# Kernel tuning notes

Measured on AMD Instinct MI355X. Metric: run time of the kernel, lower is better.

## Reference

```python
import jax, jax.numpy as jnp
import numpy as np

B, S, D, H = 4, 2048, 128, 8

def setup_inputs() -> dict:
    key = jax.random.key(0)
    ks = jax.random.split(key, 11)
    sc_in = 1.0 / np.sqrt(D)
    sc_out = 1.0 / np.sqrt(H * D)
    return {
        "Q": jax.random.normal(ks[0], (B, S, D), jnp.float32),
        "K": jax.random.normal(ks[1], (B, S, D), jnp.float32),
        "V": jax.random.normal(ks[2], (B, S, D), jnp.float32),
        "WQ_w": jax.random.normal(ks[3], (H * D, D), jnp.float32) * sc_in,
        "WQ_b": jax.random.normal(ks[4], (H * D,), jnp.float32) * 0.01,
        "WK_w": jax.random.normal(ks[5], (H * D, D), jnp.float32) * sc_in,
        "WK_b": jax.random.normal(ks[6], (H * D,), jnp.float32) * 0.01,
        "WV_w": jax.random.normal(ks[7], (H * D, D), jnp.float32) * sc_in,
        "WV_b": jax.random.normal(ks[8], (H * D,), jnp.float32) * 0.01,
        "W_w": jax.random.normal(ks[9], (D, H * D), jnp.float32) * sc_out,
        "W_b": jax.random.normal(ks[10], (D,), jnp.float32) * 0.01,
    }

def reference(Q, K, V, WQ_w, WQ_b, WK_w, WK_b, WV_w, WV_b, W_w, W_b):
    b, s, d = Q.shape
    h = WQ_w.shape[0] // d
    # Linear projections: [b,s,d] -> [b,s,h*d] -> [b,h,s,d]
    rQ = (Q @ WQ_w.T + WQ_b).reshape(b, s, h, d).transpose(0, 2, 1, 3)
    rK = (K @ WK_w.T + WK_b).reshape(b, s, h, d).transpose(0, 2, 1, 3)
    rV = (V @ WV_w.T + WV_b).reshape(b, s, h, d).transpose(0, 2, 1, 3)
    # Scores: [b,h,s,s], scaled by sqrt(head_dim) = sqrt(input_dim)
    scores = jnp.einsum("bhqd,bhkd->bhqk", rQ, rK) / jnp.sqrt(jnp.asarray(d, rQ.dtype))
    sim = jax.nn.softmax(scores, axis=-1)
    # Attend and merge heads: [b,h,s,d] -> [b,s,h*d]
    oV = jnp.einsum("bhqk,bhkd->bqhd", sim, rV).reshape(b, s, h * d)
    return oV @ W_w.T + W_b
```

## Files before the change

### kernel.cpp

```cpp
#include <hip/hip_runtime.h>
#include <hip/hip_bf16.h>

typedef unsigned short u16;
typedef unsigned int   u32;
typedef short v8s __attribute__((ext_vector_type(8)));
typedef float v4f __attribute__((ext_vector_type(4)));
typedef float v16f __attribute__((ext_vector_type(16)));
typedef int   v2i __attribute__((ext_vector_type(2)));

#define MFMA16(a,b,c) __builtin_amdgcn_mfma_f32_16x16x32_bf16(a,b,c,0,0,0)
#define MFMA32(a,b,c) __builtin_amdgcn_mfma_f32_32x32x16_bf16(a,b,c,0,0,0)


__device__ __forceinline__ u16 f2b(float f){ u32 i; __builtin_memcpy(&i,&f,4); u32 r = (i + 0x7FFFu + ((i>>16)&1u))>>16; return (u16)r; }
__device__ __forceinline__ u32 pk2(float a, float b){
  __hip_bfloat162 h = __float22bfloat162_rn(make_float2(a,b));
  u32 r; __builtin_memcpy(&r,&h,4); return r;
}

__device__ __forceinline__ void gl16(const void* g, void* l){
  __builtin_amdgcn_global_load_lds((const __attribute__((address_space(1))) u32*)g,
                                   (__attribute__((address_space(3))) u32*)l, 16, 0, 0);
}

__device__ __forceinline__ void stage8f(const float* g, u16* l){
  float4 a = *(const float4*)g, b = *(const float4*)(g+4);
  uint4 q;
  q.x = pk2(a.x, a.y); q.y = pk2(a.z, a.w);
  q.z = pk2(b.x, b.y); q.w = pk2(b.z, b.w);
  *(uint4*)l = q;
}

__global__ __launch_bounds__(256) void proj_qkv(
    const float* __restrict__ Qx, const float* __restrict__ Kx, const float* __restrict__ Vx,
    const float* __restrict__ WQw, const float* __restrict__ WQb,
    const float* __restrict__ WKw, const float* __restrict__ WKb,
    const float* __restrict__ WVw, const float* __restrict__ WVb,
    u16* __restrict__ Qp, u16* __restrict__ Kp, u16* __restrict__ Vt)
{
  __shared__ u16 smem[32768];
  u16* As = smem;
  u16* Ws = smem + 16384;

  const int z = blockIdx.z;
  const float* X    = (z==0) ? Qx  : (z==1 ? Kx  : Vx);
  const float* W    = (z==0) ? WQw : (z==1 ? WKw : WVw);
  const float* bias = (z==0) ? WQb : (z==1 ? WKb : WVb);
  u16* out          = (z==0) ? Qp  : (z==1 ? Kp  : Vt);
  const float qs    = (z==0) ? 0.12751743076f : 1.0f;

  const int tid = threadIdx.x, wv = tid>>6, lane = tid&63;
  const int quad = lane>>4, l16 = lane&15;
  const int r4 = lane>>2, c4 = lane&3;
  const int m0 = blockIdx.x*128, n0 = blockIdx.y*128;

  for (int idx = wv; idx < 32; idx += 4) {
    int kt = idx >> 3, rg = idx & 7;
    int row = rg*16 + r4;
    stage8f(X + (size_t)(m0+row)*128 + kt*32 + c4*8, &As[kt*4096 + rg*512 + lane*8]);
    stage8f(W + (size_t)(n0+row)*128 + kt*32 + c4*8, &Ws[kt*4096 + rg*512 + lane*8]);
  }
  __syncthreads();

  const int wm = wv & 1, wn = wv >> 1;
  v4f acc[4][4];
#pragma unroll
  for (int i=0;i<4;i++)
#pragma unroll
    for (int j=0;j<4;j++) acc[i][j] = (v4f){0.f,0.f,0.f,0.f};

  if (z < 2) {
#pragma unroll
    for (int ks=0; ks<4; ++ks) {
      v8s af[4], bf[4];
#pragma unroll
      for (int mi=0; mi<4; ++mi) af[mi] = *(const v8s*)&As[ks*4096 + (wm*64+mi*16+l16)*32 + quad*8];
#pragma unroll
      for (int ni=0; ni<4; ++ni) bf[ni] = *(const v8s*)&Ws[ks*4096 + (wn*64+ni*16+l16)*32 + quad*8];
#pragma unroll
      for (int mi=0; mi<4; ++mi)
#pragma unroll
        for (int ni=0; ni<4; ++ni)
          acc[mi][ni] = MFMA16(bf[ni], af[mi], acc[mi][ni]);
    }
    __syncthreads();
    u16* Cs = smem;
#pragma unroll
    for (int ni=0; ni<4; ++ni) {
      int nl = wn*64 + ni*16 + quad*4;
      int nb = n0 + nl;
      float bv0 = bias[nb+0]*qs;
      float bv1 = bias[nb+1]*qs;
      float bv2 = bias[nb+2]*qs;
      float bv3 = bias[nb+3]*qs;
#pragma unroll
      for (int mi=0; mi<4; ++mi) {
        int ml = wm*64 + mi*16 + l16;
        uint2 pk;
        pk.x = pk2(fmaf(acc[mi][ni][0], qs, bv0), fmaf(acc[mi][ni][1], qs, bv1));
        pk.y = pk2(fmaf(acc[mi][ni][2], qs, bv2), fmaf(acc[mi][ni][3], qs, bv3));
        *(uint2*)&Cs[ml*136 + nl] = pk;
      }
    }
    __syncthreads();
    const int h = n0 >> 7;
    const int b = m0 >> 11, s0 = m0 & 2047;
    u16* gout = out + (((size_t)((b<<3) + h)*2048 + s0) << 7);
#pragma unroll
    for (int j = 0; j < 8; ++j) {
      int off = wv*8192 + j*1024 + lane*16;
      int row = off >> 8;
      int col = (off >> 1) & 127;
      *(uint4*)&gout[(size_t)row*128 + col] = *(const uint4*)&Cs[row*136 + col];
    }
  } else {
#pragma unroll
    for (int ks=0; ks<4; ++ks) {
      v8s af[4], bf[4];
#pragma unroll
      for (int mi=0; mi<4; ++mi) af[mi] = *(const v8s*)&As[ks*4096 + (wm*64+mi*16+l16)*32 + quad*8];
#pragma unroll
      for (int ni=0; ni<4; ++ni) bf[ni] = *(const v8s*)&Ws[ks*4096 + (wn*64+ni*16+l16)*32 + quad*8];
#pragma unroll
      for (int mi=0; mi<4; ++mi)
#pragma unroll
        for (int ni=0; ni<4; ++ni)
          acc[mi][ni] = MFMA16(af[mi], bf[ni], acc[mi][ni]);
    }
    __syncthreads();
    u16* Cs = smem;
#pragma unroll
    for (int ni=0; ni<4; ++ni) {
      int nl = wn*64 + ni*16 + l16;
      float bv = bias[n0 + nl];
#pragma unroll
      for (int mi=0; mi<4; ++mi) {
        int ml = wm*64 + mi*16 + quad*4;
        uint2 pk;
        pk.x = pk2(acc[mi][ni][0] + bv, acc[mi][ni][1] + bv);
        pk.y = pk2(acc[mi][ni][2] + bv, acc[mi][ni][3] + bv);
        *(uint2*)&Cs[nl*136 + ml] = pk;
      }
    }
    __syncthreads();
    const int nl = tid >> 1;
    const int mb = (tid & 1) * 64;
    const int h = (n0 + nl) >> 7, dh = (n0 + nl) & 127;
    const int b = m0 >> 11, s0 = m0 & 2047;
    size_t gbase = (((size_t)((b<<3) + h)*128 + dh)*2048) + s0 + mb;
    size_t lbase = (size_t)nl*136 + mb;
#pragma unroll
    for (int j = 0; j < 8; ++j)
      *(uint4*)&out[gbase + j*8] = *(const uint4*)&Cs[lbase + j*8];
  }
}

__global__ __launch_bounds__(256, 2) void attn(
    const u16* __restrict__ Qp, const u16* __restrict__ Kp,
    const u16* __restrict__ Vt, u16* __restrict__ O)
{
  __shared__ u16 smem[32768];

  const int tid = threadIdx.x, wv = tid>>6, lane = tid&63;
  const int l32 = lane&31, h = lane>>5;

  const int n  = blockIdx.x;
  const int bh = (n&7)*4 + (n>>7);
  const int q0 = ((n>>3)&15) * 128;

  const u16* Qb = Qp + (size_t)bh*262144 + (size_t)q0*128;
  const u16* Kb = Kp + (size_t)bh*262144;
  const u16* Vb = Vt + (size_t)bh*262144;

  for (int r = 0; r < 8; ++r) {
    int idx = r*256 + tid;
    int kd = idx>>8, q = (idx>>1)&127, hh = idx&1;
    gl16(Qb + q*128 + kd*16 + hh*8, &smem[idx*8]);
  }
  __syncthreads();
  const int qrow = wv*32 + l32;
  v8s qf[8];
#pragma unroll
  for (int kd = 0; kd < 8; ++kd)
    qf[kd] = *(const v8s*)&smem[kd*2048 + qrow*16 + h*8];
  __syncthreads();

  int gK[4], gV[4], lK[4], lV[4];
#pragma unroll
  for (int r = 0; r < 4; ++r) {
    int idx = r*256 + tid;
    lK[r] = idx*8;  lV[r] = 16384 + idx*8;
    int key = idx>>4, pcK = idx&15;
    gK[r] = key*128 + ((pcK ^ (key&15)))*8;
    int d = idx>>3, pcV = idx&7;
    gV[r] = d*2048 + ((pcV ^ (d&7)))*8;
  }
  int kfo[8], vfo[4];
#pragma unroll
  for (int kd = 0; kd < 8; ++kd) kfo[kd] = ((kd*2 + h) ^ (l32 & 15)) * 8;
#pragma unroll
  for (int kt = 0; kt < 4; ++kt) vfo[kt] = ((kt*2 + h) ^ (l32 & 7)) * 8;

  v8s onesf;
#pragma unroll
  for (int j = 0; j < 8; ++j) onesf[j] = (short)0x3F80;

  v16f oacc[4], lacc;
#pragma unroll
  for (int nt = 0; nt < 4; ++nt)
#pragma unroll
    for (int j = 0; j < 16; ++j) oacc[nt][j] = 0.f;
#pragma unroll
  for (int j = 0; j < 16; ++j) lacc[j] = 0.f;

#pragma unroll
  for (int r = 0; r < 4; ++r) gl16(Kb + gK[r], &smem[lK[r]]);
#pragma unroll
  for (int r = 0; r < 4; ++r) gl16(Vb + gV[r], &smem[lV[r]]);

  for (int it = 0; it < 32; ++it) {
    const int cur = it & 1;
    const int ko = cur*8192;
    const int vo = cur*8192;
    __syncthreads();

    if (it + 1 < 32) {
      const u16* Kt  = Kb + (it+1)*8192;
      const u16* Vtt = Vb + (it+1)*64;
      const int po = (cur^1)*8192;
#pragma unroll
      for (int r = 0; r < 4; ++r) gl16(Kt  + gK[r], &smem[po + lK[r]]);
#pragma unroll
      for (int r = 0; r < 4; ++r) gl16(Vtt + gV[r], &smem[po + lV[r] - 16384 + 16384]);
    }

    v16f sa[2];
#pragma unroll
    for (int m = 0; m < 2; ++m)
#pragma unroll
      for (int j = 0; j < 16; ++j) sa[m][j] = 0.f;
    __builtin_amdgcn_s_setprio(1);
#pragma unroll
    for (int kd = 0; kd < 8; ++kd) {
#pragma unroll
      for (int m = 0; m < 2; ++m) {
        v8s kf = *(const v8s*)&smem[ko + (m*32 + l32)*128 + kfo[kd]];
        sa[m] = MFMA32(kf, qf[kd], sa[m]);
      }
    }
    __builtin_amdgcn_s_setprio(0);

    u32 P32[2][4][2];
#pragma unroll
    for (int m = 0; m < 2; ++m)
#pragma unroll
      for (int g = 0; g < 4; ++g) {
        P32[m][g][0] = pk2(__builtin_amdgcn_exp2f(sa[m][g*4+0]),
                           __builtin_amdgcn_exp2f(sa[m][g*4+1]));
        P32[m][g][1] = pk2(__builtin_amdgcn_exp2f(sa[m][g*4+2]),
                           __builtin_amdgcn_exp2f(sa[m][g*4+3]));
      }

    v8s pf[4];
#pragma unroll
    for (int kt = 0; kt < 4; ++kt) {
      const int m = kt >> 1, e = (kt & 1) * 2, o = e + 1;
      union { u32 u[4]; v8s s; } f;
#if __has_builtin(__builtin_amdgcn_permlane32_swap)
      v2i r0 = __builtin_amdgcn_permlane32_swap((int)P32[m][e][0], (int)P32[m][o][0], false, false);
      v2i r1 = __builtin_amdgcn_permlane32_swap((int)P32[m][e][1], (int)P32[m][o][1], false, false);
      f.u[0] = (u32)r0[0]; f.u[1] = (u32)r1[0];
      f.u[2] = (u32)r0[1]; f.u[3] = (u32)r1[1];
#else
      u32 a0 = P32[m][e][0], b0 = P32[m][o][0];
      u32 a1 = P32[m][e][1], b1 = P32[m][o][1];
      asm("v_permlane32_swap_b32 %0, %1" : "+v"(a0), "+v"(b0));
      asm("v_permlane32_swap_b32 %0, %1" : "+v"(a1), "+v"(b1));
      f.u[0] = a0; f.u[1] = a1; f.u[2] = b0; f.u[3] = b1;
#endif
      pf[kt] = f.s;
    }

    __builtin_amdgcn_s_setprio(1);
#pragma unroll
    for (int kt = 0; kt < 4; ++kt) {
      lacc = MFMA32(pf[kt], onesf, lacc);
#pragma unroll
      for (int nt = 0; nt < 4; ++nt) {
        v8s vf = *(const v8s*)&smem[16384 + vo + (nt*32 + l32)*64 + vfo[kt]];
        oacc[nt] = MFMA32(pf[kt], vf, oacc[nt]);
      }
    }
    __builtin_amdgcn_s_setprio(0);
  }

  const int b = bh >> 3, hd = bh & 7;
#pragma unroll
  for (int reg = 0; reg < 16; ++reg) {
    int q = q0 + wv*32 + (reg&3) + 8*(reg>>2) + 4*h;
    float inv = 1.0f / lacc[reg];
    size_t base = ((size_t)(b*2048 + q))*1024 + hd*128;
#pragma unroll
    for (int nt = 0; nt < 4; ++nt)
      O[base + nt*32 + l32] = f2b(oacc[nt][reg] * inv);
  }
}

__global__ __launch_bounds__(256) void outproj(
    const u16* __restrict__ A, const float* __restrict__ Ww,
    const float* __restrict__ Wb, float* __restrict__ out)
{
  __shared__ u16 As[2][2048];
  __shared__ u16 Ws[2][8192];

  const int tid = threadIdx.x, wv = tid>>6, lane = tid&63;
  const int quad = lane>>4, l16 = lane&15;
  const int r4 = lane>>2, c4 = lane&3;
  const int m0 = blockIdx.x*32;

  v4f acc[2][2];
#pragma unroll
  for (int i=0;i<2;i++)
#pragma unroll
    for (int j=0;j<2;j++) acc[i][j] = (v4f){0.f,0.f,0.f,0.f};

  auto stage = [&](int kb, int buf) {
    {
      int kt = wv >> 1, rg = wv & 1;
      int row = rg*16 + r4;
      gl16(A + (size_t)(m0+row)*1024 + kb + kt*32 + c4*8, &As[buf][kt*1024 + rg*512 + lane*8]);
    }
    for (int idx = wv; idx < 16; idx += 4) {
      int kt = idx >> 3, rg = idx & 7;
      int row = rg*16 + r4;
      stage8f(Ww + (size_t)row*1024 + kb + kt*32 + c4*8, &Ws[buf][kt*4096 + rg*512 + lane*8]);
    }
  };

  stage(0, 0);
  for (int kb = 0; kb < 1024; kb += 64) {
    const int cur = (kb >> 6) & 1;
    __syncthreads();
    if (kb + 64 < 1024) stage(kb + 64, cur ^ 1);
#pragma unroll
    for (int ks = 0; ks < 2; ++ks) {
      v8s af0 = *(const v8s*)&As[cur][ks*1024 + (l16)*32 + quad*8];
      v8s af1 = *(const v8s*)&As[cur][ks*1024 + (16 + l16)*32 + quad*8];
#pragma unroll
      for (int nj = 0; nj < 2; ++nj) {
        v8s bf = *(const v8s*)&Ws[cur][ks*4096 + ((wv*2+nj)*16 + l16)*32 + quad*8];
        acc[0][nj] = MFMA16(af0, bf, acc[0][nj]);
        acc[1][nj] = MFMA16(af1, bf, acc[1][nj]);
      }
    }
  }

#pragma unroll
  for (int nj = 0; nj < 2; ++nj) {
    int col = (wv*2+nj)*16 + l16;
    float bv = Wb[col];
#pragma unroll
    for (int mi = 0; mi < 2; ++mi) {
#pragma unroll
      for (int r = 0; r < 4; ++r) {
        int row = m0 + mi*16 + quad*4 + r;
        out[(size_t)row*128 + col] = acc[mi][nj][r] + bv;
      }
    }
  }
}

extern "C" void kernel_launch(void* const* d_in, const int* in_sizes, int n_in,
                              void* d_out, int out_size, void* d_ws, size_t ws_size,
                              hipStream_t stream) {
  const float* Q   = (const float*)d_in[0];
  const float* K   = (const float*)d_in[1];
  const float* V   = (const float*)d_in[2];
  const float* WQw = (const float*)d_in[3];
  const float* WQb = (const float*)d_in[4];
  const float* WKw = (const float*)d_in[5];
  const float* WKb = (const float*)d_in[6];
  const float* WVw = (const float*)d_in[7];
  const float* WVb = (const float*)d_in[8];
  const float* Ww  = (const float*)d_in[9];
  const float* Wb  = (const float*)d_in[10];
  u16* ws = (u16*)d_ws;

  const size_t SZ = (size_t)4*8*2048*128;
  u16* Qp = ws;
  u16* Kp = Qp + SZ;
  u16* Vt = Kp + SZ;
  u16* Ow = Vt + SZ;

  hipLaunchKernelGGL(proj_qkv, dim3(64,8,3), dim3(256), 0, stream,
                     Q,K,V,WQw,WQb,WKw,WKb,WVw,WVb,Qp,Kp,Vt);
  hipLaunchKernelGGL(attn, dim3(512), dim3(256), 0, stream, Qp,Kp,Vt,Ow);
  hipLaunchKernelGGL(outproj, dim3(256), dim3(256), 0, stream, Ow, Ww, Wb, (float*)d_out);
}
```

Before: 211.5 us.

## Split-K the output projection across four blocks with a separate reduction kernel

The output projection grid grows from 256 to 1024 blocks, each covering a quarter of the 1024-wide K dimension and writing fp32 partial sums into workspace. A new reduction kernel adds the four partials plus the bias into the final output. The aim is to fill more compute units than the original 256-block launch could. The cost is an extra launch and about 16 MB of partial-sum traffic. The partials reuse the start of the workspace where Qp/Kp sit, which are already consumed by attention by then.

New measurement: 192.7 us. -8.9%, faster.

```diff
diff --git a/kernel.cpp b/kernel.cpp
--- a/kernel.cpp
+++ b/kernel.cpp
@@ -308,7 +308,7 @@
 
 __global__ __launch_bounds__(256) void outproj(
     const u16* __restrict__ A, const float* __restrict__ Ww,
-    const float* __restrict__ Wb, float* __restrict__ out)
+    float* __restrict__ P)
 {
   __shared__ u16 As[2][2048];
   __shared__ u16 Ws[2][8192];
@@ -316,7 +316,8 @@
   const int tid = threadIdx.x, wv = tid>>6, lane = tid&63;
   const int quad = lane>>4, l16 = lane&15;
   const int r4 = lane>>2, c4 = lane&3;
-  const int m0 = blockIdx.x*32;
+  const int m0 = (blockIdx.x >> 2) * 32;
+  const int k0 = (blockIdx.x & 3) * 256;
 
   v4f acc[2][2];
 #pragma unroll
@@ -328,20 +329,20 @@
     {
       int kt = wv >> 1, rg = wv & 1;
       int row = rg*16 + r4;
-      gl16(A + (size_t)(m0+row)*1024 + kb + kt*32 + c4*8, &As[buf][kt*1024 + rg*512 + lane*8]);
+      gl16(A + (size_t)(m0+row)*1024 + k0 + kb + kt*32 + c4*8, &As[buf][kt*1024 + rg*512 + lane*8]);
     }
     for (int idx = wv; idx < 16; idx += 4) {
       int kt = idx >> 3, rg = idx & 7;
       int row = rg*16 + r4;
-      stage8f(Ww + (size_t)row*1024 + kb + kt*32 + c4*8, &Ws[buf][kt*4096 + rg*512 + lane*8]);
+      stage8f(Ww + (size_t)row*1024 + k0 + kb + kt*32 + c4*8, &Ws[buf][kt*4096 + rg*512 + lane*8]);
     }
   };
 
   stage(0, 0);
-  for (int kb = 0; kb < 1024; kb += 64) {
+  for (int kb = 0; kb < 256; kb += 64) {
     const int cur = (kb >> 6) & 1;
     __syncthreads();
-    if (kb + 64 < 1024) stage(kb + 64, cur ^ 1);
+    if (kb + 64 < 256) stage(kb + 64, cur ^ 1);
 #pragma unroll
     for (int ks = 0; ks < 2; ++ks) {
       v8s af0 = *(const v8s*)&As[cur][ks*1024 + (l16)*32 + quad*8];
@@ -355,19 +356,37 @@
     }
   }
 
+  float* out = P + (size_t)(blockIdx.x & 3) * 1048576;
 #pragma unroll
   for (int nj = 0; nj < 2; ++nj) {
     int col = (wv*2+nj)*16 + l16;
-    float bv = Wb[col];
 #pragma unroll
     for (int mi = 0; mi < 2; ++mi) {
 #pragma unroll
       for (int r = 0; r < 4; ++r) {
         int row = m0 + mi*16 + quad*4 + r;
-        out[(size_t)row*128 + col] = acc[mi][nj][r] + bv;
-      }
-    }
-  }
+        out[(size_t)row*128 + col] = acc[mi][nj][r];
+      }
+    }
+  }
+}
+
+__global__ __launch_bounds__(256) void outred(
+    const float* __restrict__ P, const float* __restrict__ Wb,
+    float* __restrict__ out)
+{
+  int i0 = (blockIdx.x*256 + threadIdx.x)*4;
+  float4 a = *(const float4*)&P[i0];
+  float4 b = *(const float4*)&P[1048576 + i0];
+  float4 c = *(const float4*)&P[2097152 + i0];
+  float4 d = *(const float4*)&P[3145728 + i0];
+  float4 bv = *(const float4*)&Wb[i0 & 127];
+  float4 r;
+  r.x = a.x + b.x + c.x + d.x + bv.x;
+  r.y = a.y + b.y + c.y + d.y + bv.y;
+  r.z = a.z + b.z + c.z + d.z + bv.z;
+  r.w = a.w + b.w + c.w + d.w + bv.w;
+  *(float4*)&out[i0] = r;
 }
 
 extern "C" void kernel_launch(void* const* d_in, const int* in_sizes, int n_in,
@@ -391,9 +410,11 @@
   u16* Kp = Qp + SZ;
   u16* Vt = Kp + SZ;
   u16* Ow = Vt + SZ;
+  float* Pp = (float*)ws;
 
   hipLaunchKernelGGL(proj_qkv, dim3(64,8,3), dim3(256), 0, stream,
                      Q,K,V,WQw,WQb,WKw,WKb,WVw,WVb,Qp,Kp,Vt);
   hipLaunchKernelGGL(attn, dim3(512), dim3(256), 0, stream, Qp,Kp,Vt,Ow);
-  hipLaunchKernelGGL(outproj, dim3(256), dim3(256), 0, stream, Ow, Ww, Wb, (float*)d_out);
-}
+  hipLaunchKernelGGL(outproj, dim3(1024), dim3(256), 0, stream, Ow, Ww, Pp);
+  hipLaunchKernelGGL(outred, dim3(1024), dim3(256), 0, stream, Pp, Wb, (float*)d_out);
+}
```
